# Performance work log

Hardware: AMD Instinct MI355X
Metric: run time of the kernel (lower is better)

## Reference

```python
import jax, jax.numpy as jnp
import numpy as np

N, E, IN, H, C, T = 50000, 800000, 128, 64, 64, 2
F1, FO1 = H, H // T   # conv1: per-tower in/out feats
F2, FO2 = H, C // T   # conv2
STD_EPS = 1e-5
BN_EPS = 1e-5


def setup_inputs() -> dict:
    key = jax.random.key(0)
    ks = jax.random.split(key, 12)
    rn = lambda k, s, sc=0.05: jax.random.normal(k, s, jnp.float32) * sc
    return {
        "x": jax.random.normal(ks[0], (N, IN), jnp.float32),
        "embed_W": rn(ks[1], (IN, H)),
        "embed_b": jnp.zeros((H,), jnp.float32),
        "pre_W1": rn(ks[2], (T, 2 * F1, F1)),
        "pre_b1": jnp.zeros((T, F1), jnp.float32),
        "post_W1": rn(ks[3], (T, 13 * F1, FO1)),
        "post_b1": jnp.zeros((T, FO1), jnp.float32),
        "lin_W1": rn(ks[4], (H, H)),
        "lin_b1": jnp.zeros((H,), jnp.float32),
        "bn_gamma": jnp.ones((H,), jnp.float32),
        "bn_beta": jnp.zeros((H,), jnp.float32),
        "pre_W2": rn(ks[5], (T, 2 * F2, F2)),
        "pre_b2": jnp.zeros((T, F2), jnp.float32),
        "post_W2": rn(ks[6], (T, 13 * F2, FO2)),
        "post_b2": jnp.zeros((T, FO2), jnp.float32),
        "lin_W2": rn(ks[7], (C, C)),
        "lin_b2": jnp.zeros((C,), jnp.float32),
        "src": jax.random.randint(ks[8], (E,), 0, N, jnp.int32),
        "dst": jax.random.randint(ks[9], (E,), 0, N, jnp.int32),
    }


def _pna_conv(h, src, dst, deg_raw, degc, avg_log, preW, preb, postW, postb, linW, linb):
    # h: [N, F] node feats; messages flow src -> dst, aggregated at dst.
    m = jnp.concatenate([h[dst], h[src]], axis=-1)            # [E, 2F]  (cat[x_i, x_j])
    m = jnp.einsum('ef,tfg->etg', m, preW) + preb[None]       # [E, T, F] per-tower pre-NN
    seg = lambda v: jax.ops.segment_sum(v, dst, num_segments=N)
    cnt = degc[:, None, None]                                 # clamped degree >= 1
    has = (deg_raw > 0)[:, None, None]
    mean = seg(m) / cnt                                       # [N, T, F]
    mean_sq = seg(m * m) / cnt
    mn = jnp.where(has, jax.ops.segment_min(m, dst, num_segments=N), 0.0)
    mx = jnp.where(has, jax.ops.segment_max(m, dst, num_segments=N), 0.0)
    std = jnp.sqrt(jax.nn.relu(mean_sq - mean * mean) + STD_EPS)
    agg = jnp.concatenate([mean, mn, mx, std], axis=-1)       # [N, T, 4F]
    ld = jnp.log(degc + 1.0)[:, None, None]
    out = jnp.concatenate([agg, agg * (ld / avg_log), agg * (avg_log / ld)], axis=-1)  # [N, T, 12F]
    F = h.shape[-1]
    out = jnp.concatenate([jnp.broadcast_to(h[:, None, :], (N, T, F)), out], axis=-1)  # [N, T, 13F]
    out = jnp.einsum('ntf,tfg->ntg', out, postW) + postb[None]  # [N, T, FO] per-tower post-NN
    return out.reshape(N, -1) @ linW + linb                    # final mixing Linear(out, out)


def reference(x, embed_W, embed_b, pre_W1, pre_b1, post_W1, post_b1, lin_W1, lin_b1,
              bn_gamma, bn_beta, pre_W2, pre_b2, post_W2, post_b2, lin_W2, lin_b2,
              src, dst):
    deg_raw = jax.ops.segment_sum(jnp.ones((E,), jnp.float32), dst, num_segments=N)
    degc = jnp.maximum(deg_raw, 1.0)
    avg_log = jnp.mean(jnp.log(deg_raw + 1.0))  # avg_deg['log'] from the graph's degrees
    h = x @ embed_W + embed_b
    h = _pna_conv(h, src, dst, deg_raw, degc, avg_log,
                  pre_W1, pre_b1, post_W1, post_b1, lin_W1, lin_b1)
    mu = jnp.mean(h, axis=0)
    var = jnp.mean((h - mu) ** 2, axis=0)
    h = bn_gamma * (h - mu) / jnp.sqrt(var + BN_EPS) + bn_beta
    h = jax.nn.relu(h)  # dropout is identity in eval mode
    return _pna_conv(h, src, dst, deg_raw, degc, avg_log,
                     pre_W2, pre_b2, post_W2, post_b2, lin_W2, lin_b2)
```

## Files before the change

### kernel.cpp

```cpp
#include <hip/hip_runtime.h>
#include <hip/hip_fp16.h>

#define N_NODES 50000
#define E_EDGES 800000
#define IN_F    128
#define H_F     64
#define STD_EPS 1e-5f
#define BN_EPS  1e-5f

#define HIST_BLK 3125
#define EMB_BLK  768
#define SCAN_BLK 49
#define TRANS_BLK 448

typedef __attribute__((ext_vector_type(8))) short bf16x8;
typedef __attribute__((ext_vector_type(4))) float f32x4;

__device__ __forceinline__ unsigned bf16_rne(float f) {
  unsigned u = __float_as_uint(f);
  return (u + 0x7fffu + ((u >> 16) & 1u)) >> 16;
}
__device__ __forceinline__ void bf16_split2(float x, float y, unsigned& hi, unsigned& lo) {
  unsigned hx = bf16_rne(x), hy = bf16_rne(y);
  float rx = x - __uint_as_float(hx << 16);
  float ry = y - __uint_as_float(hy << 16);
  hi = hx | (hy << 16);
  lo = bf16_rne(rx) | (bf16_rne(ry) << 16);
}

#define MFMA(acc, a, b) acc = __builtin_amdgcn_mfma_f32_16x16x32_bf16(a, b, acc, 0, 0, 0)

__global__ __launch_bounds__(256) void k_hist_embed(const int* __restrict__ dst,
                                                    int* __restrict__ deg,
                                                    const float* __restrict__ x,
                                                    const float* __restrict__ W,
                                                    const float* __restrict__ bias,
                                                    float* __restrict__ h) {
  __shared__ float sW[IN_F * 64];
  __shared__ float sx[IN_F * 36];
  if (blockIdx.x < HIST_BLK) {
    int e = blockIdx.x * 256 + threadIdx.x;
    atomicAdd(&deg[dst[e]], 1);
    return;
  }
  for (int i = threadIdx.x; i < IN_F * 64; i += 256) sW[i] = W[i];
  int f = threadIdx.x & 63, ng = threadIdx.x >> 6;
  float bj = bias[f];
  const int NGRP = (N_NODES + 31) / 32;
  for (int grp = blockIdx.x - HIST_BLK; grp < NGRP; grp += EMB_BLK) {
    int n0 = grp * 32;
    __syncthreads();
    for (int idx = threadIdx.x; idx < 32 * IN_F; idx += 256) {
      int nl = idx >> 7, k = idx & 127;
      int n = n0 + nl;
      sx[k * 36 + nl] = (n < N_NODES) ? x[(size_t)n * IN_F + k] : 0.f;
    }
    __syncthreads();
    float a[8] = {bj, bj, bj, bj, bj, bj, bj, bj};
    const float* xp = &sx[ng * 8];
#pragma unroll 4
    for (int k = 0; k < IN_F; k++) {
      float4 h0 = *(const float4*)&xp[k * 36];
      float4 h1 = *(const float4*)&xp[k * 36 + 4];
      float w = sW[k * 64 + f];
      a[0] = fmaf(h0.x, w, a[0]); a[1] = fmaf(h0.y, w, a[1]);
      a[2] = fmaf(h0.z, w, a[2]); a[3] = fmaf(h0.w, w, a[3]);
      a[4] = fmaf(h1.x, w, a[4]); a[5] = fmaf(h1.y, w, a[5]);
      a[6] = fmaf(h1.z, w, a[6]); a[7] = fmaf(h1.w, w, a[7]);
    }
#pragma unroll
    for (int j = 0; j < 8; j++) {
      int n = n0 + ng * 8 + j;
      if (n < N_NODES) h[(size_t)n * 64 + f] = a[j];
    }
  }
}

__global__ __launch_bounds__(256) void k_scanpart_trans(const int* __restrict__ deg,
                                                        int* __restrict__ partials,
                                                        float* __restrict__ scalars,
                                                        const float* __restrict__ pW1,
                                                        const float* __restrict__ pW2,
                                                        const float* __restrict__ lW1,
                                                        const float* __restrict__ lW2,
                                                        unsigned short* __restrict__ WBhi,
                                                        unsigned short* __restrict__ WBlo,
                                                        float* __restrict__ lWT) {
  __shared__ int red[256];
  __shared__ float redf[256];
  if (blockIdx.x < SCAN_BLK) {
    int base = blockIdx.x * 1024;
    int s = 0; float ls = 0.f;
    for (int j = threadIdx.x; j < 1024; j += 256) {
      int i = base + j;
      if (i < N_NODES) { int d = deg[i]; s += d; ls += logf((float)d + 1.0f); }
    }
    red[threadIdx.x] = s; redf[threadIdx.x] = ls; __syncthreads();
    for (int st = 128; st > 0; st >>= 1) {
      if (threadIdx.x < st) {
        red[threadIdx.x] += red[threadIdx.x + st];
        redf[threadIdx.x] += redf[threadIdx.x + st];
      }
      __syncthreads();
    }
    if (threadIdx.x == 0) {
      partials[blockIdx.x] = red[0];
      atomicAdd(&scalars[0], redf[0]);
    }
    return;
  }
  int idx = (blockIdx.x - SCAN_BLK) * 256 + threadIdx.x;
  if (idx < 106496) {
    int f = idx % 832;
    int rest = idx / 832;
    int col = rest & 31, tt = rest >> 5;
    const float* srcp = (tt >= 2) ? pW2 : pW1;
    float v = srcp[((size_t)(tt & 1) * 832 + f) * 32 + col];
    unsigned hb = bf16_rne(v);
    float rsd = v - __uint_as_float(hb << 16);
    WBhi[idx] = (unsigned short)hb;
    WBlo[idx] = (unsigned short)bf16_rne(rsd);
  } else if (idx < 114688) {
    int jj = idx - 106496;
    int layer = jj / 4096, r2 = jj % 4096;
    int c4 = r2 / 256, r3 = r2 % 256;
    int col = r3 / 4, j = r3 % 4;
    const float* srcl = layer ? lW2 : lW1;
    lWT[jj] = srcl[(c4 * 4 + j) * 64 + col];
  }
}

__global__ __launch_bounds__(256) void k_scan_final(const int* __restrict__ deg,
                                                    const int* __restrict__ partials,
                                                    int* __restrict__ row_ptr,
                                                    int* __restrict__ cursor,
                                                    float* __restrict__ scalars) {
  __shared__ int ts[256];
  __shared__ int sbase;
  if (threadIdx.x == 0) {
    int pre = 0;
    for (int b = 0; b < (int)blockIdx.x; b++) pre += partials[b];
    sbase = pre;
    if (blockIdx.x == 0) {
      scalars[1] = scalars[0] / (float)N_NODES;
      row_ptr[N_NODES] = E_EDGES;
    }
  }
  int base = blockIdx.x * 1024 + threadIdx.x * 4;
  int d[4]; int s = 0;
#pragma unroll
  for (int j = 0; j < 4; j++) {
    int i = base + j;
    d[j] = (i < N_NODES) ? deg[i] : 0;
    s += d[j];
  }
  ts[threadIdx.x] = s; __syncthreads();
  for (int off = 1; off < 256; off <<= 1) {
    int t = (threadIdx.x >= off) ? ts[threadIdx.x - off] : 0;
    __syncthreads();
    ts[threadIdx.x] += t;
    __syncthreads();
  }
  int excl = (threadIdx.x > 0) ? ts[threadIdx.x - 1] : 0;
  int run = sbase + excl;
#pragma unroll
  for (int j = 0; j < 4; j++) {
    int i = base + j;
    if (i < N_NODES) { row_ptr[i] = run; cursor[i] = run; run += d[j]; }
  }
}

__global__ __launch_bounds__(256) void k_scatter(const int* __restrict__ src,
                                                 const int* __restrict__ dst,
                                                 int* __restrict__ cursor,
                                                 int* __restrict__ csr_src) {
  int e = blockIdx.x * 256 + threadIdx.x;
  if (e < E_EDGES) {
    int d = dst[e];
    int p = atomicAdd(&cursor[d], 1);
    csr_src[p] = src[e];
  }
}

template <bool BN>
__global__ __launch_bounds__(256) void k_preab(const float* __restrict__ hin,
                                               const float* __restrict__ preW,
                                               const float* __restrict__ preb,
                                               const float* __restrict__ bnsum,
                                               const float* __restrict__ bnsumsq,
                                               const float* __restrict__ gamma,
                                               const float* __restrict__ beta,
                                               float* __restrict__ h2out,
                                               float* __restrict__ hA,
                                               __half* __restrict__ hB) {
  __shared__ float sWp[64 * 128];
  __shared__ float sh[64 * 68];
  __shared__ float sbn[128];
  int t = blockIdx.x & 1;
  const float* Wsrc = preW + (size_t)t * 128 * 64;
  for (int i = threadIdx.x; i < 64 * 64; i += 256) {
    int k = i >> 6, f = i & 63;
    float wa = Wsrc[k * 64 + f];
    float wb = Wsrc[(64 + k) * 64 + f];
    *(float2*)&sWp[k * 128 + f * 2] = make_float2(wa, wb);
  }
  if (BN && threadIdx.x < 64) {
    int c = threadIdx.x;
    float mu = bnsum[c] * (1.f / N_NODES);
    float var = bnsumsq[c] * (1.f / N_NODES) - mu * mu;
    float sc = gamma[c] / sqrtf(var + BN_EPS);
    sbn[c] = sc;
    sbn[64 + c] = fmaf(-mu, sc, beta[c]);
  }
  int f = threadIdx.x & 63, ng = threadIdx.x >> 6;
  float pb = preb[t * 64 + f];
  int nblk2 = gridDim.x >> 1;
  const int NGRP = (N_NODES + 63) / 64;
  for (int grp = blockIdx.x >> 1; grp < NGRP; grp += nblk2) {
    int n0 = grp * 64;
    __syncthreads();
    for (int idx = threadIdx.x; idx < 64 * 64; idx += 256) {
      int nl = idx >> 6, k = idx & 63;
      int n = n0 + nl;
      float v = 0.f;
      if (n < N_NODES) {
        v = hin[(size_t)n * 64 + k];
        if (BN) {
          v = fmaxf(fmaf(v, sbn[k], sbn[64 + k]), 0.f);
          if (t == 0) h2out[(size_t)n * 64 + k] = v;
        }
      }
      sh[k * 68 + nl] = v;
    }
    __syncthreads();
    float a[16], b[16];
#pragma unroll
    for (int j = 0; j < 16; j++) { a[j] = pb; b[j] = 0.f; }
    const float* hp = &sh[ng * 16];
    const float* wp = &sWp[f * 2];
#pragma unroll 2
    for (int k = 0; k < 64; k++) {
      float4 h0 = *(const float4*)&hp[k * 68];
      float4 h1 = *(const float4*)&hp[k * 68 + 4];
      float4 h2 = *(const float4*)&hp[k * 68 + 8];
      float4 h3 = *(const float4*)&hp[k * 68 + 12];
      float2 w2 = *(const float2*)&wp[k * 128];
      a[0]  = fmaf(h0.x, w2.x, a[0]);  b[0]  = fmaf(h0.x, w2.y, b[0]);
      a[1]  = fmaf(h0.y, w2.x, a[1]);  b[1]  = fmaf(h0.y, w2.y, b[1]);
      a[2]  = fmaf(h0.z, w2.x, a[2]);  b[2]  = fmaf(h0.z, w2.y, b[2]);
      a[3]  = fmaf(h0.w, w2.x, a[3]);  b[3]  = fmaf(h0.w, w2.y, b[3]);
      a[4]  = fmaf(h1.x, w2.x, a[4]);  b[4]  = fmaf(h1.x, w2.y, b[4]);
      a[5]  = fmaf(h1.y, w2.x, a[5]);  b[5]  = fmaf(h1.y, w2.y, b[5]);
      a[6]  = fmaf(h1.z, w2.x, a[6]);  b[6]  = fmaf(h1.z, w2.y, b[6]);
      a[7]  = fmaf(h1.w, w2.x, a[7]);  b[7]  = fmaf(h1.w, w2.y, b[7]);
      a[8]  = fmaf(h2.x, w2.x, a[8]);  b[8]  = fmaf(h2.x, w2.y, b[8]);
      a[9]  = fmaf(h2.y, w2.x, a[9]);  b[9]  = fmaf(h2.y, w2.y, b[9]);
      a[10] = fmaf(h2.z, w2.x, a[10]); b[10] = fmaf(h2.z, w2.y, b[10]);
      a[11] = fmaf(h2.w, w2.x, a[11]); b[11] = fmaf(h2.w, w2.y, b[11]);
      a[12] = fmaf(h3.x, w2.x, a[12]); b[12] = fmaf(h3.x, w2.y, b[12]);
      a[13] = fmaf(h3.y, w2.x, a[13]); b[13] = fmaf(h3.y, w2.y, b[13]);
      a[14] = fmaf(h3.z, w2.x, a[14]); b[14] = fmaf(h3.z, w2.y, b[14]);
      a[15] = fmaf(h3.w, w2.x, a[15]); b[15] = fmaf(h3.w, w2.y, b[15]);
    }
    int tf = t * 64 + f;
#pragma unroll
    for (int j = 0; j < 16; j++) {
      int n = n0 + ng * 16 + j;
      if (n < N_NODES) {
        hA[(size_t)n * 128 + tf] = a[j];
        hB[(size_t)n * 128 + tf] = __float2half(b[j]);
      }
    }
  }
}

__global__ __launch_bounds__(256, 6) void k_conv(const float* __restrict__ hA,
                                                 const __half* __restrict__ hB,
                                                 const float* __restrict__ hskip,
                                                 const int* __restrict__ row_ptr,
                                                 const int* __restrict__ csr_src,
                                                 const unsigned short* __restrict__ WBhi,
                                                 const unsigned short* __restrict__ WBlo,
                                                 const float* __restrict__ postb,
                                                 const float* __restrict__ linWT,
                                                 const float* __restrict__ linb,
                                                 const float* __restrict__ scalars,
                                                 float* __restrict__ out) {
  __shared__ unsigned sAhi[2688];
  __shared__ unsigned sAlo[2688];
  __shared__ float sAB[16];
  int w = threadIdx.x >> 6, lane = threadIdx.x & 63;
  int n0 = blockIdx.x * 8;
  int t = lane >> 5, fb2 = (lane & 31) * 2;
  int off = t * 64 + fb2;
  float avg = scalars[1];

#pragma unroll 1
  for (int k = 0; k < 2; k++) {
    int nl = w * 2 + k;
    int n = n0 + nl;
    float2 a = *(const float2*)&hA[(size_t)n * 128 + off];
    int rp0 = __builtin_amdgcn_readfirstlane(row_ptr[n]);
    int rp1 = __builtin_amdgcn_readfirstlane(row_ptr[n + 1]);
    int dg = rp1 - rp0;
    float sx0=0,sy0=0,qx0=0,qy0=0, sx1=0,sy1=0,qx1=0,qy1=0;
    float mnx0=INFINITY,mny0=INFINITY,mxx0=-INFINITY,mxy0=-INFINITY;
    float mnx1=INFINITY,mny1=INFINITY,mxx1=-INFINITY,mxy1=-INFINITY;
    int nloop = dg >> 3;
    if (nloop > 0) {
      int b = rp0;
      int s0=csr_src[b],s1=csr_src[b+1],s2=csr_src[b+2],s3=csr_src[b+3],
          s4=csr_src[b+4],s5=csr_src[b+5],s6=csr_src[b+6],s7=csr_src[b+7];
      __half2 qa0 = *(const __half2*)&hB[(size_t)s0 * 128 + off];
      __half2 qa1 = *(const __half2*)&hB[(size_t)s1 * 128 + off];
      __half2 qa2 = *(const __half2*)&hB[(size_t)s2 * 128 + off];
      __half2 qa3 = *(const __half2*)&hB[(size_t)s3 * 128 + off];
      __half2 qa4 = *(const __half2*)&hB[(size_t)s4 * 128 + off];
      __half2 qa5 = *(const __half2*)&hB[(size_t)s5 * 128 + off];
      __half2 qa6 = *(const __half2*)&hB[(size_t)s6 * 128 + off];
      __half2 qa7 = *(const __half2*)&hB[(size_t)s7 * 128 + off];
      for (int it = 0; ; it++) {
        bool more = (it + 1 < nloop);
        __half2 qb0, qb1, qb2, qb3, qb4, qb5, qb6, qb7;
        if (more) {
          int c = rp0 + ((it + 1) << 3);
          s0=csr_src[c];s1=csr_src[c+1];s2=csr_src[c+2];s3=csr_src[c+3];
          s4=csr_src[c+4];s5=csr_src[c+5];s6=csr_src[c+6];s7=csr_src[c+7];
          qb0 = *(const __half2*)&hB[(size_t)s0 * 128 + off];
          qb1 = *(const __half2*)&hB[(size_t)s1 * 128 + off];
          qb2 = *(const __half2*)&hB[(size_t)s2 * 128 + off];
          qb3 = *(const __half2*)&hB[(size_t)s3 * 128 + off];
          qb4 = *(const __half2*)&hB[(size_t)s4 * 128 + off];
          qb5 = *(const __half2*)&hB[(size_t)s5 * 128 + off];
          qb6 = *(const __half2*)&hB[(size_t)s6 * 128 + off];
          qb7 = *(const __half2*)&hB[(size_t)s7 * 128 + off];
        }
        float2 v0 = __half22float2(qa0), v1 = __half22float2(qa1);
        float2 v2 = __half22float2(qa2), v3 = __half22float2(qa3);
        float2 v4 = __half22float2(qa4), v5 = __half22float2(qa5);
        float2 v6 = __half22float2(qa6), v7 = __half22float2(qa7);
        sx0 += v0.x; qx0 = fmaf(v0.x,v0.x,qx0); mnx0 = fminf(mnx0,v0.x); mxx0 = fmaxf(mxx0,v0.x);
        sy0 += v0.y; qy0 = fmaf(v0.y,v0.y,qy0); mny0 = fminf(mny0,v0.y); mxy0 = fmaxf(mxy0,v0.y);
        sx1 += v1.x; qx1 = fmaf(v1.x,v1.x,qx1); mnx1 = fminf(mnx1,v1.x); mxx1 = fmaxf(mxx1,v1.x);
        sy1 += v1.y; qy1 = fmaf(v1.y,v1.y,qy1); mny1 = fminf(mny1,v1.y); mxy1 = fmaxf(mxy1,v1.y);
        sx0 += v2.x; qx0 = fmaf(v2.x,v2.x,qx0); mnx0 = fminf(mnx0,v2.x); mxx0 = fmaxf(mxx0,v2.x);
        sy0 += v2.y; qy0 = fmaf(v2.y,v2.y,qy0); mny0 = fminf(mny0,v2.y); mxy0 = fmaxf(mxy0,v2.y);
        sx1 += v3.x; qx1 = fmaf(v3.x,v3.x,qx1); mnx1 = fminf(mnx1,v3.x); mxx1 = fmaxf(mxx1,v3.x);
        sy1 += v3.y; qy1 = fmaf(v3.y,v3.y,qy1); mny1 = fminf(mny1,v3.y); mxy1 = fmaxf(mxy1,v3.y);
        sx0 += v4.x; qx0 = fmaf(v4.x,v4.x,qx0); mnx0 = fminf(mnx0,v4.x); mxx0 = fmaxf(mxx0,v4.x);
        sy0 += v4.y; qy0 = fmaf(v4.y,v4.y,qy0); mny0 = fminf(mny0,v4.y); mxy0 = fmaxf(mxy0,v4.y);
        sx1 += v5.x; qx1 = fmaf(v5.x,v5.x,qx1); mnx1 = fminf(mnx1,v5.x); mxx1 = fmaxf(mxx1,v5.x);
        sy1 += v5.y; qy1 = fmaf(v5.y,v5.y,qy1); mny1 = fminf(mny1,v5.y); mxy1 = fmaxf(mxy1,v5.y);
        sx0 += v6.x; qx0 = fmaf(v6.x,v6.x,qx0); mnx0 = fminf(mnx0,v6.x); mxx0 = fmaxf(mxx0,v6.x);
        sy0 += v6.y; qy0 = fmaf(v6.y,v6.y,qy0); mny0 = fminf(mny0,v6.y); mxy0 = fmaxf(mxy0,v6.y);
        sx1 += v7.x; qx1 = fmaf(v7.x,v7.x,qx1); mnx1 = fminf(mnx1,v7.x); mxx1 = fmaxf(mxx1,v7.x);
        sy1 += v7.y; qy1 = fmaf(v7.y,v7.y,qy1); mny1 = fminf(mny1,v7.y); mxy1 = fmaxf(mxy1,v7.y);
        if (!more) break;
        qa0=qb0; qa1=qb1; qa2=qb2; qa3=qb3; qa4=qb4; qa5=qb5; qa6=qb6; qa7=qb7;
      }
    }
    {
      int i = rp0 + (nloop << 3);
      int r = rp1 - i;
      if (r > 0) {
        int sj[7];
#pragma unroll
        for (int j = 0; j < 7; j++) sj[j] = csr_src[i + (j < r ? j : r - 1)];
        __half2 hq[7];
#pragma unroll
        for (int j = 0; j < 7; j++) hq[j] = *(const __half2*)&hB[(size_t)sj[j] * 128 + off];
#pragma unroll
        for (int j = 0; j < 7; j++) {
          if (j < r) {
            float2 v = __half22float2(hq[j]);
            if (j & 1) {
              sx1 += v.x; qx1 = fmaf(v.x,v.x,qx1); mnx1 = fminf(mnx1,v.x); mxx1 = fmaxf(mxx1,v.x);
              sy1 += v.y; qy1 = fmaf(v.y,v.y,qy1); mny1 = fminf(mny1,v.y); mxy1 = fmaxf(mxy1,v.y);
            } else {
              sx0 += v.x; qx0 = fmaf(v.x,v.x,qx0); mnx0 = fminf(mnx0,v.x); mxx0 = fmaxf(mxx0,v.x);
              sy0 += v.y; qy0 = fmaf(v.y,v.y,qy0); mny0 = fminf(mny0,v.y); mxy0 = fmaxf(mxy0,v.y);
            }
          }
        }
      }
    }
    float cnt = (float)(dg > 0 ? dg : 1);
    float inv = 1.0f / cnt;
    float mrx = (sx0 + sx1) * inv, mry = (sy0 + sy1) * inv;
    float sdx = sqrtf(fmaxf((qx0 + qx1) * inv - mrx * mrx, 0.f) + STD_EPS);
    float sdy = sqrtf(fmaxf((qy0 + qy1) * inv - mry * mry, 0.f) + STD_EPS);
    float mnx = fminf(mnx0, mnx1), mny = fminf(mny0, mny1);
    float mxx = fmaxf(mxx0, mxx1), mxy = fmaxf(mxy0, mxy1);
    float ax = a.x, ay = a.y;
    if (dg == 0) { mnx = 0; mny = 0; mxx = 0; mxy = 0; ax = 0; ay = 0; }
    float meanx = mrx + ax, meany = mry + ay;
    mnx += ax; mny += ay; mxx += ax; mxy += ay;
    float ldv = logf(cnt + 1.f);
    float2 hsv = *(const float2*)&hskip[(size_t)n * 64 + fb2];
    unsigned* ahp = &sAhi[(t * 8 + nl) * 168 + (fb2 >> 1)];
    unsigned* alp = &sAlo[(t * 8 + nl) * 168 + (fb2 >> 1)];
    unsigned hi, lo;
    bf16_split2(hsv.x, hsv.y, hi, lo);   ahp[0]   = hi; alp[0]   = lo;
    bf16_split2(meanx, meany, hi, lo);   ahp[32]  = hi; alp[32]  = lo;
    bf16_split2(mnx, mny, hi, lo);       ahp[64]  = hi; alp[64]  = lo;
    bf16_split2(mxx, mxy, hi, lo);       ahp[96]  = hi; alp[96]  = lo;
    bf16_split2(sdx, sdy, hi, lo);       ahp[128] = hi; alp[128] = lo;
    if (lane == 0) { sAB[nl] = ldv / avg; sAB[8 + nl] = avg / ldv; }
  }
  __syncthreads();

  f32x4 acc1 = {0.f, 0.f, 0.f, 0.f};
  f32x4 acc2 = {0.f, 0.f, 0.f, 0.f};
  f32x4 acc3 = {0.f, 0.f, 0.f, 0.f};
  int tw = w >> 1, ntile = w & 1;
  int kq = lane >> 4;
  {
    const bf16x8* Ah = (const bf16x8*)sAhi + (tw * 8 + (lane & 7)) * 42 + kq;
    const bf16x8* Al = (const bf16x8*)sAlo + (tw * 8 + (lane & 7)) * 42 + kq;
    int brow = (tw * 32 + ntile * 16 + (lane & 15)) * 104 + kq;
    const bf16x8* Bh = (const bf16x8*)WBhi + brow;
    const bf16x8* Bl = (const bf16x8*)WBlo + brow;
    bf16x8 bh_0 = Bh[0], bl_0 = Bl[0];
    bf16x8 bh_1 = Bh[4], bl_1 = Bl[4];
#pragma unroll
    for (int s = 0; s < 10; s++) {
      bf16x8 bh_n, bl_n;
      if (s < 8) { bh_n = Bh[(s + 2) * 4]; bl_n = Bl[(s + 2) * 4]; }
      bf16x8 ah = Ah[s * 4], al = Al[s * 4];
      MFMA(acc1, ah, bh_0); MFMA(acc1, al, bh_0); MFMA(acc1, ah, bl_0);
      bh_0 = bh_1; bl_0 = bl_1; bh_1 = bh_n; bl_1 = bl_n;
    }
    bf16x8 c_0 = Bh[40], d_0 = Bh[72];
    bf16x8 c_1 = Bh[44], d_1 = Bh[76];
#pragma unroll
    for (int s = 0; s < 8; s++) {
      bf16x8 c_n, d_n;
      if (s < 6) { c_n = Bh[48 + s * 4]; d_n = Bh[80 + s * 4]; }
      bf16x8 ah = Ah[(s + 2) * 4], al = Al[(s + 2) * 4];
      MFMA(acc2, ah, c_0); MFMA(acc2, al, c_0);
      MFMA(acc3, ah, d_0); MFMA(acc3, al, d_0);
      c_0 = c_1; d_0 = d_1; c_1 = c_n; d_1 = d_n;
    }
  }
  __syncthreads();

  float* spo = (float*)sAhi;
  if (lane < 32) {
    int colg = tw * 32 + ntile * 16 + (lane & 15);
    float pbv = postb[colg];
    int rbase = kq * 4;
#pragma unroll
    for (int r = 0; r < 4; r++) {
      int nr = rbase + r;
      spo[nr * 64 + colg] = acc1[r] + sAB[nr] * acc2[r] + sAB[8 + nr] * acc3[r] + pbv;
    }
  }
  __syncthreads();

  {
    float la0 = linb[lane], la1 = la0;
    const float4* lw4 = (const float4*)linWT + lane;
    const float* p0 = &spo[(w * 2) * 64];
    const float* p1 = p0 + 64;
#pragma unroll
    for (int c4 = 0; c4 < 16; c4++) {
      float4 lwv = lw4[c4 * 64];
      float4 pa = *(const float4*)&p0[c4 * 4];
      float4 pb2 = *(const float4*)&p1[c4 * 4];
      la0 = fmaf(pa.w, lwv.w, fmaf(pa.z, lwv.z, fmaf(pa.y, lwv.y, fmaf(pa.x, lwv.x, la0))));
      la1 = fmaf(pb2.w, lwv.w, fmaf(pb2.z, lwv.z, fmaf(pb2.y, lwv.y, fmaf(pb2.x, lwv.x, la1))));
    }
    size_t ob = (size_t)(n0 + w * 2) * 64 + lane;
    out[ob] = la0;
    out[ob + 64] = la1;
  }
}

__global__ __launch_bounds__(256) void k_bnstats(const float* __restrict__ y,
                                                 float* __restrict__ bnsum,
                                                 float* __restrict__ bnsumsq) {
  __shared__ float r1[256], r2[256];
  int c = threadIdx.x & 63, r = threadIdx.x >> 6;
  float s = 0, q = 0;
  for (int n = blockIdx.x * 4 + r; n < N_NODES; n += gridDim.x * 4) {
    float v = y[(size_t)n * 64 + c];
    s += v; q = fmaf(v, v, q);
  }
  r1[threadIdx.x] = s; r2[threadIdx.x] = q; __syncthreads();
  if (threadIdx.x < 64) {
    s = r1[threadIdx.x] + r1[threadIdx.x + 64] + r1[threadIdx.x + 128] + r1[threadIdx.x + 192];
    q = r2[threadIdx.x] + r2[threadIdx.x + 64] + r2[threadIdx.x + 128] + r2[threadIdx.x + 192];
    atomicAdd(&bnsum[threadIdx.x], s);
    atomicAdd(&bnsumsq[threadIdx.x], q);
  }
}

extern "C" void kernel_launch(void* const* d_in, const int* in_sizes, int n_in,
                              void* d_out, int out_size, void* d_ws, size_t ws_size,
                              hipStream_t stream) {
  const float* x      = (const float*)d_in[0];
  const float* embW   = (const float*)d_in[1];
  const float* embB   = (const float*)d_in[2];
  const float* preW1  = (const float*)d_in[3];
  const float* preb1  = (const float*)d_in[4];
  const float* postW1 = (const float*)d_in[5];
  const float* postb1 = (const float*)d_in[6];
  const float* linW1  = (const float*)d_in[7];
  const float* linb1  = (const float*)d_in[8];
  const float* gamma  = (const float*)d_in[9];
  const float* beta   = (const float*)d_in[10];
  const float* preW2  = (const float*)d_in[11];
  const float* preb2  = (const float*)d_in[12];
  const float* postW2 = (const float*)d_in[13];
  const float* postb2 = (const float*)d_in[14];
  const float* linW2  = (const float*)d_in[15];
  const float* linb2  = (const float*)d_in[16];
  const int*   src    = (const int*)d_in[17];
  const int*   dst    = (const int*)d_in[18];
  float* out = (float*)d_out;

  char* w = (char*)d_ws;
  size_t o = 0;
  int*   deg     = (int*)(w + o);   o += (size_t)N_NODES * 4;
  float* scalars = (float*)(w + o); o += 64;
  float* bnsum   = (float*)(w + o); o += 256;
  float* bnsumsq = (float*)(w + o); o += 256;
  size_t zero_len = o;
  o = (o + 255) & ~(size_t)255;
  int* partials = (int*)(w + o);  o += 256;
  int* row_ptr  = (int*)(w + o);  o += (size_t)(N_NODES + 1) * 4; o = (o + 255) & ~(size_t)255;
  int* cursor   = (int*)(w + o);  o += (size_t)N_NODES * 4;       o = (o + 255) & ~(size_t)255;
  int* csr      = (int*)(w + o);  o += (size_t)E_EDGES * 4;       o = (o + 255) & ~(size_t)255;
  unsigned short* WBhi = (unsigned short*)(w + o); o += (size_t)2 * 53248 * 2;
  unsigned short* WBlo = (unsigned short*)(w + o); o += (size_t)2 * 53248 * 2;
  float* linWT  = (float*)(w + o); o += (size_t)2 * 4096 * 4;
  float* h1 = (float*)(w + o); o += (size_t)N_NODES * 64 * 4;
  float* y1 = (float*)(w + o); o += (size_t)N_NODES * 64 * 4;
  float* h2 = (float*)(w + o); o += (size_t)N_NODES * 64 * 4;
  float* hA = (float*)(w + o); o += (size_t)N_NODES * 128 * 4;
  __half* hBh = (__half*)(w + o); o += (size_t)N_NODES * 128 * 2;

  hipMemsetAsync(w, 0, zero_len, stream);

  k_hist_embed<<<HIST_BLK + EMB_BLK, 256, 0, stream>>>(dst, deg, x, embW, embB, h1);
  k_scanpart_trans<<<SCAN_BLK + TRANS_BLK, 256, 0, stream>>>(
      deg, partials, scalars, postW1, postW2, linW1, linW2, WBhi, WBlo, linWT);
  k_scan_final<<<SCAN_BLK, 256, 0, stream>>>(deg, partials, row_ptr, cursor, scalars);
  k_scatter<<<(E_EDGES + 255) / 256, 256, 0, stream>>>(src, dst, cursor, csr);

  k_preab<false><<<768, 256, 0, stream>>>(h1, preW1, preb1, nullptr, nullptr,
                                          nullptr, nullptr, nullptr, hA, hBh);
  k_conv<<<N_NODES / 8, 256, 0, stream>>>(hA, hBh, h1, row_ptr, csr,
                                          WBhi, WBlo, postb1, linWT, linb1, scalars, y1);
  k_bnstats<<<256, 256, 0, stream>>>(y1, bnsum, bnsumsq);
  k_preab<true><<<768, 256, 0, stream>>>(y1, preW2, preb2, bnsum, bnsumsq,
                                         gamma, beta, h2, hA, hBh);
  k_conv<<<N_NODES / 8, 256, 0, stream>>>(hA, hBh, h2, row_ptr, csr,
                                          WBhi + 53248, WBlo + 53248, postb2,
                                          linWT + 4096, linb2, scalars, out);
}
```

Baseline: 557.6 us.

## Swizzle conv LDS tiles, drop scaler LDS, raise occupancy target

The k_conv aggregation tile in LDS changes from a padded 168-word row stride to an unpadded 160-word stride with an XOR swizzle on the write and MFMA-read sides. This cuts LDS use and aims to avoid bank conflicts. The per-node degree scalers are no longer staged in shared memory; they are recomputed from row_ptr in the epilogue. The launch bound rises from 6 to 8 waves per SIMD and the hskip load is hoisted earlier. The risks are extra register pressure or spills under the tighter bound, and redundant log computations.

Result: slower. 574.9 us (+3.1%).

```diff
diff --git a/kernel.cpp b/kernel.cpp
--- a/kernel.cpp
+++ b/kernel.cpp
@@ -274,7 +274,7 @@
   }
 }
 
-__global__ __launch_bounds__(256, 6) void k_conv(const float* __restrict__ hA,
+__global__ __launch_bounds__(256, 8) void k_conv(const float* __restrict__ hA,
                                                  const __half* __restrict__ hB,
                                                  const float* __restrict__ hskip,
                                                  const int* __restrict__ row_ptr,
@@ -286,9 +286,8 @@
                                                  const float* __restrict__ linb,
                                                  const float* __restrict__ scalars,
                                                  float* __restrict__ out) {
-  __shared__ unsigned sAhi[2688];
-  __shared__ unsigned sAlo[2688];
-  __shared__ float sAB[16];
+  __shared__ unsigned sAhi[2560];
+  __shared__ unsigned sAlo[2560];
   int w = threadIdx.x >> 6, lane = threadIdx.x & 63;
   int n0 = blockIdx.x * 8;
   int t = lane >> 5, fb2 = (lane & 31) * 2;
@@ -300,6 +299,7 @@
     int nl = w * 2 + k;
     int n = n0 + nl;
     float2 a = *(const float2*)&hA[(size_t)n * 128 + off];
+    float2 hsv = *(const float2*)&hskip[(size_t)n * 64 + fb2];
     int rp0 = __builtin_amdgcn_readfirstlane(row_ptr[n]);
     int rp1 = __builtin_amdgcn_readfirstlane(row_ptr[n + 1]);
     int dg = rp1 - rp0;
@@ -395,17 +395,16 @@
     if (dg == 0) { mnx = 0; mny = 0; mxx = 0; mxy = 0; ax = 0; ay = 0; }
     float meanx = mrx + ax, meany = mry + ay;
     mnx += ax; mny += ay; mxx += ax; mxy += ay;
-    float ldv = logf(cnt + 1.f);
-    float2 hsv = *(const float2*)&hskip[(size_t)n * 64 + fb2];
-    unsigned* ahp = &sAhi[(t * 8 + nl) * 168 + (fb2 >> 1)];
-    unsigned* alp = &sAlo[(t * 8 + nl) * 168 + (fb2 >> 1)];
+    unsigned* ahp = &sAhi[(t * 8 + nl) * 160];
+    unsigned* alp = &sAlo[(t * 8 + nl) * 160];
+    int sw = (nl & 3) << 2;
+    int p = lane & 31;
     unsigned hi, lo;
-    bf16_split2(hsv.x, hsv.y, hi, lo);   ahp[0]   = hi; alp[0]   = lo;
-    bf16_split2(meanx, meany, hi, lo);   ahp[32]  = hi; alp[32]  = lo;
-    bf16_split2(mnx, mny, hi, lo);       ahp[64]  = hi; alp[64]  = lo;
-    bf16_split2(mxx, mxy, hi, lo);       ahp[96]  = hi; alp[96]  = lo;
-    bf16_split2(sdx, sdy, hi, lo);       ahp[128] = hi; alp[128] = lo;
-    if (lane == 0) { sAB[nl] = ldv / avg; sAB[8 + nl] = avg / ldv; }
+    bf16_split2(hsv.x, hsv.y, hi, lo);   ahp[p ^ sw]         = hi; alp[p ^ sw]         = lo;
+    bf16_split2(meanx, meany, hi, lo);   ahp[(p + 32) ^ sw]  = hi; alp[(p + 32) ^ sw]  = lo;
+    bf16_split2(mnx, mny, hi, lo);       ahp[(p + 64) ^ sw]  = hi; alp[(p + 64) ^ sw]  = lo;
+    bf16_split2(mxx, mxy, hi, lo);       ahp[(p + 96) ^ sw]  = hi; alp[(p + 96) ^ sw]  = lo;
+    bf16_split2(sdx, sdy, hi, lo);       ahp[(p + 128) ^ sw] = hi; alp[(p + 128) ^ sw] = lo;
   }
   __syncthreads();
 
@@ -415,8 +414,9 @@
   int tw = w >> 1, ntile = w & 1;
   int kq = lane >> 4;
   {
-    const bf16x8* Ah = (const bf16x8*)sAhi + (tw * 8 + (lane & 7)) * 42 + kq;
-    const bf16x8* Al = (const bf16x8*)sAlo + (tw * 8 + (lane & 7)) * 42 + kq;
+    const bf16x8* Ah = (const bf16x8*)(sAhi + (tw * 8 + (lane & 7)) * 160);
+    const bf16x8* Al = (const bf16x8*)(sAlo + (tw * 8 + (lane & 7)) * 160);
+    int kqs = kq ^ (lane & 3);
     int brow = (tw * 32 + ntile * 16 + (lane & 15)) * 104 + kq;
     const bf16x8* Bh = (const bf16x8*)WBhi + brow;
     const bf16x8* Bl = (const bf16x8*)WBlo + brow;
@@ -426,7 +426,7 @@
     for (int s = 0; s < 10; s++) {
       bf16x8 bh_n, bl_n;
       if (s < 8) { bh_n = Bh[(s + 2) * 4]; bl_n = Bl[(s + 2) * 4]; }
-      bf16x8 ah = Ah[s * 4], al = Al[s * 4];
+      bf16x8 ah = Ah[s * 4 + kqs], al = Al[s * 4 + kqs];
       MFMA(acc1, ah, bh_0); MFMA(acc1, al, bh_0); MFMA(acc1, ah, bl_0);
       bh_0 = bh_1; bl_0 = bl_1; bh_1 = bh_n; bl_1 = bl_n;
     }
@@ -436,7 +436,7 @@
     for (int s = 0; s < 8; s++) {
       bf16x8 c_n, d_n;
       if (s < 6) { c_n = Bh[48 + s * 4]; d_n = Bh[80 + s * 4]; }
-      bf16x8 ah = Ah[(s + 2) * 4], al = Al[(s + 2) * 4];
+      bf16x8 ah = Ah[(s + 2) * 4 + kqs], al = Al[(s + 2) * 4 + kqs];
       MFMA(acc2, ah, c_0); MFMA(acc2, al, c_0);
       MFMA(acc3, ah, d_0); MFMA(acc3, al, d_0);
       c_0 = c_1; d_0 = d_1; c_1 = c_n; d_1 = d_n;
@@ -449,10 +449,16 @@
     int colg = tw * 32 + ntile * 16 + (lane & 15);
     float pbv = postb[colg];
     int rbase = kq * 4;
+    int rb = n0 + rbase;
+    int p0 = row_ptr[rb], p1 = row_ptr[rb+1], p2 = row_ptr[rb+2],
+        p3 = row_ptr[rb+3], p4 = row_ptr[rb+4];
+    int dgv[4] = {p1 - p0, p2 - p1, p3 - p2, p4 - p3};
 #pragma unroll
     for (int r = 0; r < 4; r++) {
-      int nr = rbase + r;
-      spo[nr * 64 + colg] = acc1[r] + sAB[nr] * acc2[r] + sAB[8 + nr] * acc3[r] + pbv;
+      float cnt = (float)(dgv[r] > 0 ? dgv[r] : 1);
+      float ldv = logf(cnt + 1.f);
+      spo[(rbase + r) * 64 + colg] =
+          acc1[r] + (ldv / avg) * acc2[r] + (avg / ldv) * acc3[r] + pbv;
     }
   }
   __syncthreads();
```
